# Kernel tuning notes

Hardware: AMD Instinct MI355X
Metric: run time of the kernel (lower is better)

The kernel has to match this reference:

```python
import jax, jax.numpy as jnp
import numpy as np

S = 16384   # num src nodes
D = 16384   # num dst nodes
FS = 128    # src feature len
FD = 128    # dst feature len
R = 50.0    # dist threshold (m)
L = 2005.0  # box side so avg degree ~ 32
LN_EPS = 1e-5


def setup_inputs() -> dict:
    rng = np.random.default_rng(0)
    src_pos_np = rng.uniform(0.0, L, (S, 2)).astype(np.float32)
    dst_pos_np = rng.uniform(0.0, L, (D, 2)).astype(np.float32)
    # radius-graph edge construction (data-dependent, done once outside jit)
    es, ed = [], []
    CH = 2048
    for i in range(0, S, CH):
        d = np.linalg.norm(src_pos_np[i:i + CH, None, :] - dst_pos_np[None, :, :], axis=-1)
        si, di = np.nonzero(d <= R)
        es.append((si + i).astype(np.int32))
        ed.append(di.astype(np.int32))
    edge_src_idx = jnp.asarray(np.concatenate(es))
    edge_dst_idx = jnp.asarray(np.concatenate(ed))

    key = jax.random.key(0)
    ks = jax.random.split(key, 12)
    w = lambda k, shape: (jax.random.normal(k, shape, jnp.float32) * 0.02)
    return {
        'src_node_features': jax.random.normal(ks[0], (S, FS), jnp.float32),
        'src_node_pos': jnp.asarray(src_pos_np),
        'dst_node_features': jax.random.normal(ks[1], (D, FD), jnp.float32),
        'dst_node_pos': jnp.asarray(dst_pos_np),
        'src_w': w(ks[2], (FS, FS)), 'src_b': jnp.zeros((FS,), jnp.float32),
        'dst_w': w(ks[3], (FD, FD)), 'dst_b': jnp.zeros((FD,), jnp.float32),
        'dist_w': w(ks[4], (2, FD)), 'dist_b': jnp.zeros((FD,), jnp.float32),
        'edge_w1': w(ks[5], (FS + FD + FD, FD)), 'edge_b1': jnp.zeros((FD,), jnp.float32),
        'edge_w2': w(ks[6], (FD, FD)), 'edge_b2': jnp.zeros((FD,), jnp.float32),
        'ln_g': jnp.ones((FD,), jnp.float32), 'ln_b': jnp.zeros((FD,), jnp.float32),
        'out_w': w(ks[7], (FD, FD)), 'out_b': jnp.zeros((FD,), jnp.float32),
        'edge_src_idx': edge_src_idx,
        'edge_dst_idx': edge_dst_idx,
    }


def reference(src_node_features, src_node_pos, dst_node_features, dst_node_pos,
              src_w, src_b, dst_w, dst_b, dist_w, dist_b,
              edge_w1, edge_b1, edge_w2, edge_b2, ln_g, ln_b, out_w, out_b,
              edge_src_idx, edge_dst_idx):
    # node encoders: Linear + ReLU
    src_enc = jax.nn.relu(src_node_features @ src_w + src_b)   # [S, FS]
    dst_enc = jax.nn.relu(dst_node_features @ dst_w + dst_b)   # [D, FD]
    # gather per-edge
    e_src = src_enc[edge_src_idx]                               # [E, FS]
    e_dst = dst_enc[edge_dst_idx]                               # [E, FD]
    e_dpos = src_node_pos[edge_src_idx] - dst_node_pos[edge_dst_idx]  # [E, 2]
    e_dist = jax.nn.relu(e_dpos @ dist_w + dist_b)              # [E, FD]
    # edge MLP: Linear-ReLU-Linear on concat [E, FS+FD+FD]
    e_in = jnp.concatenate([e_src, e_dist, e_dst], axis=-1)
    e_out = jax.nn.relu(e_in @ edge_w1 + edge_b1) @ edge_w2 + edge_b2  # [E, FD]
    # scatter-add to destination nodes
    agg = dst_enc + jax.ops.segment_sum(e_out, edge_dst_idx, num_segments=D)
    # LayerNorm + ReLU + Linear + residual + ReLU
    mu = jnp.mean(agg, axis=-1, keepdims=True)
    var = jnp.mean(jnp.square(agg - mu), axis=-1, keepdims=True)
    ln = (agg - mu) * jax.lax.rsqrt(var + LN_EPS) * ln_g + ln_b
    h = jax.nn.relu(ln) @ out_w + out_b + dst_node_features
    return jax.nn.relu(h)
```

## Files before the change

### kernel.cpp

```cpp
#include <hip/hip_runtime.h>

typedef unsigned short ushort_t;
typedef unsigned int uint_t;
typedef short bhalf8 __attribute__((ext_vector_type(8)));
typedef float f32x4 __attribute__((ext_vector_type(4)));

#define DEG_CAP 96
#define PWIN 192

__device__ __forceinline__ float b2f(ushort_t u) {
    union { uint_t i; float f; } v; v.i = ((uint_t)u) << 16; return v.f;
}
__device__ __forceinline__ float u2f(uint_t u) {
    union { uint_t i; float f; } v; v.i = u; return v.f;
}
__device__ __forceinline__ ushort_t f2b(float f) {
    union { float f; uint_t i; } v; v.f = f;
    uint_t r = v.i + 0x7fffu + ((v.i >> 16) & 1u);
    return (ushort_t)(r >> 16);
}
__device__ __forceinline__ uint_t f2u(float f) {
    union { float f; uint_t i; } v; v.f = f; return v.i;
}
__device__ __forceinline__ uint_t pack_trunc(float lo, float hi) {
    return (f2u(lo) >> 16) | (f2u(hi) & 0xffff0000u);
}
__device__ __forceinline__ uint_t addpack_trunc(uint_t a, uint_t b) {
    union { uint_t i; float f; } t0, t1, s0, s1;
    t0.i = a << 16;          s0.i = b << 16;
    t1.i = a & 0xffff0000u;  s1.i = b & 0xffff0000u;
    return pack_trunc(t0.f + s0.f, t1.f + s1.f);
}

__global__ __launch_bounds__(256) void prep_kernel(
    const float* __restrict__ wsrc, const float* __restrict__ wdst,
    const float* __restrict__ w2,   const float* __restrict__ wout,
    const float* __restrict__ w1,
    ushort_t* __restrict__ msrc, ushort_t* __restrict__ mdst,
    ushort_t* __restrict__ m2,   ushort_t* __restrict__ mout,
    ushort_t* __restrict__ m1a,  ushort_t* __restrict__ m1b,
    ushort_t* __restrict__ m1c,
    const int* __restrict__ esi, const int* __restrict__ edi, int E,
    int* __restrict__ deg, int* __restrict__ bucket,
    float* __restrict__ hsum, int countB, int zeroB, int Dn)
{
    int b = blockIdx.x, tid = threadIdx.x;
    if (b < 56) {
        const float* ins[7] = { wsrc, wdst, w2, wout, w1, w1 + 16384, w1 + 32768 };
        ushort_t* outs[7]   = { msrc, mdst, m2, mout, m1a, m1b, m1c };
        int mat = b >> 3;
        const float* in = ins[mat];
        ushort_t* out = outs[mat];
        int flat = (b & 7)*256 + tid;
        int nt = flat >> 8, rem = flat & 255;
        int ks = rem >> 6, lane = rem & 63;
        int q = lane >> 4, m = lane & 15;
        #pragma unroll
        for (int j = 0; j < 8; ++j)
            out[flat*8 + j] = f2b(in[(ks*32 + q*8 + j)*128 + nt*16 + m]);
    } else if (b < 56 + countB) {
        int i = (b - 56)*256 + tid;
        if (i < E) {
            int d = edi[i];
            int p = atomicAdd(&deg[d], 1);
            if (p < DEG_CAP) bucket[(size_t)d*DEG_CAP + p] = esi[i];
        }
    } else {
        int zb = b - 56 - countB;
        float4* h4 = (float4*)hsum;
        int total4 = Dn*32;
        for (int i = zb*256 + tid; i < total4; i += zeroB*256)
            h4[i] = make_float4(0.f, 0.f, 0.f, 0.f);
    }
}

__global__ __launch_bounds__(256) void enc2_kernel(
    const float* __restrict__ src_feat, const float* __restrict__ dst_feat,
    const ushort_t* __restrict__ msrc, const ushort_t* __restrict__ mdst,
    const ushort_t* __restrict__ m1a,  const ushort_t* __restrict__ m1c,
    const float* __restrict__ src_b,   const float* __restrict__ dst_b,
    const float* __restrict__ b1,
    ushort_t* __restrict__ Csrc, ushort_t* __restrict__ Cdst,
    ushort_t* __restrict__ dst_enc,
    const int* __restrict__ deg, int* __restrict__ P,
    int* __restrict__ tileStart, int nTiles, int Dn,
    int Sb, int Db)
{
    int tid = threadIdx.x, blk = blockIdx.x;

    if (blk == Sb + Db) {
        __shared__ int sums[256];
        int per = Dn >> 8;
        const int4* d4 = (const int4*)(deg + tid*per);
        int4 v[16]; int s = 0;
        #pragma unroll
        for (int k = 0; k < 16; ++k) {
            v[k] = d4[k];
            v[k].x = min(v[k].x, DEG_CAP); v[k].y = min(v[k].y, DEG_CAP);
            v[k].z = min(v[k].z, DEG_CAP); v[k].w = min(v[k].w, DEG_CAP);
            s += v[k].x + v[k].y + v[k].z + v[k].w;
        }
        sums[tid] = s;
        __syncthreads();
        for (int off = 1; off < 256; off <<= 1) {
            int x = (tid >= off) ? sums[tid - off] : 0;
            __syncthreads();
            sums[tid] += x;
            __syncthreads();
        }
        int run = sums[tid] - s;
        int4* n4 = (int4*)(P + tid*per);
        auto wt = [&](int start, int end, int d) {
            for (int tt = (start + 63) >> 6; tt*64 < end && tt < nTiles; ++tt)
                tileStart[tt] = d;
        };
        #pragma unroll
        for (int k = 0; k < 16; ++k) {
            int d0 = tid*per + k*4;
            int4 o; int st;
            st = run; o.x = run; run += v[k].x; wt(st, run, d0 + 0);
            st = run; o.y = run; run += v[k].y; wt(st, run, d0 + 1);
            st = run; o.z = run; run += v[k].z; wt(st, run, d0 + 2);
            st = run; o.w = run; run += v[k].w; wt(st, run, d0 + 3);
            n4[k] = o;
        }
        return;
    }

    __shared__ ushort_t A_l[64*136];
    __shared__ ushort_t E_l[64*136];
    __shared__ float b_l[128];
    __shared__ float b2_l[128];

    const float* A; const ushort_t *W1m, *W2m; const float* bias; const float* bias2;
    ushort_t *outC, *outEnc; int rowbase;
    if (blk < Sb) { A = src_feat; W1m = msrc; W2m = m1a; bias = src_b;
                    outC = Csrc; outEnc = nullptr; rowbase = blk*64; bias2 = nullptr; }
    else          { A = dst_feat; W1m = mdst; W2m = m1c; bias = dst_b;
                    outC = Cdst; outEnc = dst_enc; rowbase = (blk - Sb)*64; bias2 = b1; }

    const float4* A4 = (const float4*)A;
    for (int i = tid; i < 2048; i += 256) {
        int r = i >> 5, c = i & 31;
        float4 v = A4[(size_t)(rowbase + r)*32 + c];
        uint2 u;
        u.x = pack_trunc(v.x, v.y);
        u.y = pack_trunc(v.z, v.w);
        *(uint2*)(A_l + r*136 + c*4) = u;
    }
    if (tid < 128) { b_l[tid] = bias[tid]; b2_l[tid] = bias2 ? bias2[tid] : 0.f; }
    __syncthreads();

    int lane = tid & 63, w = tid >> 6, q = lane >> 4, m = lane & 15;
    const bhalf8* Wv1 = (const bhalf8*)W1m;
    f32x4 acc[4][2] = {};
    #pragma unroll
    for (int ks = 0; ks < 4; ++ks) {
        bhalf8 bf0 = Wv1[((2*w)*4 + ks)*64 + lane];
        bhalf8 bf1 = Wv1[((2*w+1)*4 + ks)*64 + lane];
        #pragma unroll
        for (int mt = 0; mt < 4; ++mt) {
            bhalf8 a = *(const bhalf8*)(A_l + (mt*16 + m)*136 + ks*32 + q*8);
            acc[mt][0] = __builtin_amdgcn_mfma_f32_16x16x32_bf16(a, bf0, acc[mt][0], 0, 0, 0);
            acc[mt][1] = __builtin_amdgcn_mfma_f32_16x16x32_bf16(a, bf1, acc[mt][1], 0, 0, 0);
        }
    }
    #pragma unroll
    for (int mt = 0; mt < 4; ++mt)
    #pragma unroll
    for (int nt = 0; nt < 2; ++nt)
    #pragma unroll
    for (int reg = 0; reg < 4; ++reg) {
        int col = w*32 + nt*16 + m;
        int row = mt*16 + q*4 + reg;
        E_l[row*136 + col] = f2b(fmaxf(acc[mt][nt][reg] + b_l[col], 0.f));
    }
    __syncthreads();

    if (outEnc) {
        for (int i = tid; i < 1024; i += 256) {
            int r = i >> 4, c = i & 15;
            ((uint4*)outEnc)[(size_t)(rowbase + r)*16 + c] = *(const uint4*)(E_l + r*136 + c*8);
        }
    }

    const bhalf8* Wv2 = (const bhalf8*)W2m;
    f32x4 acc2[4][2] = {};
    #pragma unroll
    for (int ks = 0; ks < 4; ++ks) {
        bhalf8 bf0 = Wv2[((2*w)*4 + ks)*64 + lane];
        bhalf8 bf1 = Wv2[((2*w+1)*4 + ks)*64 + lane];
        #pragma unroll
        for (int mt = 0; mt < 4; ++mt) {
            bhalf8 a = *(const bhalf8*)(E_l + (mt*16 + m)*136 + ks*32 + q*8);
            acc2[mt][0] = __builtin_amdgcn_mfma_f32_16x16x32_bf16(a, bf0, acc2[mt][0], 0, 0, 0);
            acc2[mt][1] = __builtin_amdgcn_mfma_f32_16x16x32_bf16(a, bf1, acc2[mt][1], 0, 0, 0);
        }
    }
    #pragma unroll
    for (int mt = 0; mt < 4; ++mt)
    #pragma unroll
    for (int nt = 0; nt < 2; ++nt)
    #pragma unroll
    for (int reg = 0; reg < 4; ++reg) {
        int col = w*32 + nt*16 + m;
        int row = mt*16 + q*4 + reg;
        A_l[row*136 + col] = f2b(acc2[mt][nt][reg] + b2_l[col]);
    }
    __syncthreads();
    for (int i = tid; i < 1024; i += 256) {
        int r = i >> 4, c = i & 15;
        ((uint4*)outC)[(size_t)(rowbase + r)*16 + c] = *(const uint4*)(A_l + r*136 + c*8);
    }
}

__global__ __launch_bounds__(512, 8) void edge_kernel(
    const ushort_t* __restrict__ Csrc, const ushort_t* __restrict__ Cdst,
    const float* __restrict__ src_pos, const float* __restrict__ dst_pos,
    const int* __restrict__ P, const int* __restrict__ tileStart,
    const int* __restrict__ bucket, int E, int Dn,
    const ushort_t* __restrict__ w1bm,
    const float* __restrict__ dist_w, const float* __restrict__ dist_b,
    float* __restrict__ hsum)
{
    __shared__ char pool[17408];
    __shared__ ushort_t G[64*136];
    __shared__ int Pw[PWIN];
    __shared__ int s_l[64], d_l[64], dofs_l[64];
    __shared__ uint_t bndmask[2];
    __shared__ float dx_l[64], dy_l[64];
    __shared__ float dw0_l[128], dw1_l[128], db_l[128];

    ushort_t* X  = (ushort_t*)pool;
    ushort_t* Hc = (ushort_t*)pool;

    int tid = threadIdx.x, blk = blockIdx.x;
    int d0 = tileStart[blk];

    if (tid < PWIN) Pw[tid] = (d0 + tid < Dn) ? P[d0 + tid] : 0x7fffffff;
    if (tid < 128) {
        dw0_l[tid] = dist_w[tid];
        dw1_l[tid] = dist_w[128 + tid];
        db_l[tid]  = dist_b[tid];
    }
    __syncthreads();

    if (tid < 64) {
        int g = blk*64 + tid;
        int s = 0, d = -1;
        float dx = 0.f, dy = 0.f;
        if (g < E) {
            int i = 0;
            while (i + 1 < PWIN && Pw[i + 1] <= g) ++i;
            int p;
            if (i == PWIN - 1) {
                int lo = d0 + PWIN - 1, hi = Dn - 1;
                while (lo < hi) {
                    int mid = (lo + hi + 1) >> 1;
                    if (P[mid] <= g) lo = mid; else hi = mid - 1;
                }
                d = lo; p = g - P[lo];
            } else {
                d = d0 + i; p = g - Pw[i];
            }
            s = bucket[(size_t)d*DEG_CAP + min(p, DEG_CAP - 1)];
            float2 sp = ((const float2*)src_pos)[s];
            float2 dp = ((const float2*)dst_pos)[d];
            dx = sp.x - dp.x; dy = sp.y - dp.y;
        }
        s_l[tid] = s; d_l[tid] = d;
        dofs_l[tid] = (d >= 0) ? d*128 : -1;
        dx_l[tid] = dx; dy_l[tid] = dy;
        int dd = d_l[tid];
        int dn = (tid < 63) ? d_l[tid + 1] : -2;
        bool bnd = ((tid & 15) == 15) || (dn != dd);
        unsigned long long mask = __ballot(bnd);
        if (tid == 0) { bndmask[0] = (uint_t)mask; bndmask[1] = (uint_t)(mask >> 32); }
    }
    __syncthreads();

    const uint4* cs4 = (const uint4*)Csrc;
    const uint4* cd4 = (const uint4*)Cdst;
    #pragma unroll
    for (int k = 0; k < 2; ++k) {
        int i = tid + k*512;
        int r = i >> 4, c = i & 15;
        uint4 a = cs4[(size_t)s_l[r]*16 + c];
        uint4 b = cd4[(size_t)max(d_l[r], 0)*16 + c];
        uint4 u;
        u.x = addpack_trunc(a.x, b.x);
        u.y = addpack_trunc(a.y, b.y);
        u.z = addpack_trunc(a.z, b.z);
        u.w = addpack_trunc(a.w, b.w);
        *(uint4*)(G + r*136 + c*8) = u;
    }
    for (int i = tid; i < 4096; i += 512) {
        int r = i >> 6, j2 = (i & 63)*2;
        float dx = dx_l[r], dy = dy_l[r];
        float v0 = fmaxf(fmaf(dx, dw0_l[j2],   fmaf(dy, dw1_l[j2],   db_l[j2])),   0.f);
        float v1 = fmaxf(fmaf(dx, dw0_l[j2+1], fmaf(dy, dw1_l[j2+1], db_l[j2+1])), 0.f);
        *(uint_t*)(X + r*136 + j2) = pack_trunc(v0, v1);
    }
    __syncthreads();

    int lane = tid & 63, w = tid >> 6, q = lane >> 4, m = lane & 15;
    f32x4 acc[4] = {};
    const bhalf8* Wv = (const bhalf8*)w1bm;
    #pragma unroll
    for (int ks = 0; ks < 4; ++ks) {
        bhalf8 bf = Wv[(w*4 + ks)*64 + lane];
        #pragma unroll
        for (int mt = 0; mt < 4; ++mt) {
            bhalf8 a = *(const bhalf8*)(X + (mt*16 + m)*136 + ks*32 + q*8);
            acc[mt] = __builtin_amdgcn_mfma_f32_16x16x32_bf16(a, bf, acc[mt], 0, 0, 0);
        }
    }
    __syncthreads();

    #pragma unroll
    for (int mt = 0; mt < 4; ++mt) {
        int col = w*16 + m;
        int row0 = mt*16 + q*4;
        uint2 u;
        u.x = pack_trunc(acc[mt][0], acc[mt][1]);
        u.y = pack_trunc(acc[mt][2], acc[mt][3]);
        *(uint2*)(Hc + col*68 + row0) = u;
    }
    __syncthreads();

    {
        int j = tid & 127, h = tid >> 7;
        uint_t mask = bndmask[h >> 1] >> ((h & 1)*16);
        const ushort_t* Hcol = Hc + j*68 + h*16;
        int rbase = h*16;
        float a = 0.f;
        #pragma unroll
        for (int k4 = 0; k4 < 4; ++k4) {
            uint2 hp = *(const uint2*)(Hcol + k4*4);
            float hv[4];
            hv[0] = u2f(hp.x << 16);
            hv[1] = u2f(hp.x & 0xffff0000u);
            hv[2] = u2f(hp.y << 16);
            hv[3] = u2f(hp.y & 0xffff0000u);
            #pragma unroll
            for (int t = 0; t < 4; ++t) {
                int r = rbase + k4*4 + t;
                float g = b2f(G[r*136 + j]);
                a += fmaxf(hv[t] + g, 0.f);
                if ((mask >> (k4*4 + t)) & 1u) {
                    int ofs = dofs_l[r];
                    if (ofs >= 0) atomicAdd(&hsum[(size_t)ofs + j], a);
                    a = 0.f;
                }
            }
        }
    }
}

__global__ __launch_bounds__(256) void aggfinal16_kernel(
    const float* __restrict__ hsum, const ushort_t* __restrict__ w2m,
    const float* __restrict__ b2, const int* __restrict__ deg,
    const ushort_t* __restrict__ dst_enc, const float* __restrict__ ln_g,
    const float* __restrict__ ln_b, const ushort_t* __restrict__ moutm,
    const float* __restrict__ out_b, const float* __restrict__ dst_feat,
    float* __restrict__ out)
{
    __shared__ ushort_t A_l[16*136];
    __shared__ ushort_t E2[16*136];
    __shared__ float ps[64], ps2[64];
    __shared__ float muv[16], invv[16];
    __shared__ float pb2[128], pg[128], plb[128], pob[128];
    __shared__ int dgl[16];

    int tid = threadIdx.x, blk = blockIdx.x;
    int lane = tid & 63, w = tid >> 6, q = lane >> 4, m = lane & 15;

    if (tid < 128) { pb2[tid] = b2[tid]; pg[tid] = ln_g[tid];
                     plb[tid] = ln_b[tid]; pob[tid] = out_b[tid]; }
    if (tid < 16) dgl[tid] = deg[blk*16 + tid];
    {
        int r = tid >> 4, c = tid & 15;
        const float4* hv4 = (const float4*)hsum;
        size_t base = (size_t)(blk*16 + r)*32 + c*2;
        float4 p0 = hv4[base], p1 = hv4[base + 1];
        uint4 u;
        u.x = pack_trunc(p0.x, p0.y);
        u.y = pack_trunc(p0.z, p0.w);
        u.z = pack_trunc(p1.x, p1.y);
        u.w = pack_trunc(p1.z, p1.w);
        *(uint4*)(A_l + r*136 + c*8) = u;
        *(uint4*)(E2 + r*136 + c*8) = ((const uint4*)dst_enc)[(size_t)(blk*16 + r)*16 + c];
    }
    __syncthreads();

    const bhalf8* Wv2 = (const bhalf8*)w2m;
    f32x4 acc[2] = {};
    #pragma unroll
    for (int ks = 0; ks < 4; ++ks) {
        bhalf8 bf0 = Wv2[((2*w)*4 + ks)*64 + lane];
        bhalf8 bf1 = Wv2[((2*w+1)*4 + ks)*64 + lane];
        bhalf8 a = *(const bhalf8*)(A_l + m*136 + ks*32 + q*8);
        acc[0] = __builtin_amdgcn_mfma_f32_16x16x32_bf16(a, bf0, acc[0], 0, 0, 0);
        acc[1] = __builtin_amdgcn_mfma_f32_16x16x32_bf16(a, bf1, acc[1], 0, 0, 0);
    }
    float y[2][4];
    #pragma unroll
    for (int nt = 0; nt < 2; ++nt)
    #pragma unroll
    for (int reg = 0; reg < 4; ++reg) {
        int col = w*32 + nt*16 + m;
        int rowl = q*4 + reg;
        y[nt][reg] = acc[nt][reg] + (float)dgl[rowl]*pb2[col] + b2f(E2[rowl*136 + col]);
    }
    float s[4], s2[4];
    #pragma unroll
    for (int reg = 0; reg < 4; ++reg) {
        s[reg]  = y[0][reg] + y[1][reg];
        s2[reg] = y[0][reg]*y[0][reg] + y[1][reg]*y[1][reg];
    }
    #pragma unroll
    for (int o = 1; o < 16; o <<= 1) {
        #pragma unroll
        for (int reg = 0; reg < 4; ++reg) {
            s[reg]  += __shfl_xor(s[reg],  o);
            s2[reg] += __shfl_xor(s2[reg], o);
        }
    }
    if (m == 0) {
        #pragma unroll
        for (int reg = 0; reg < 4; ++reg) {
            ps[(q*4 + reg)*4 + w]  = s[reg];
            ps2[(q*4 + reg)*4 + w] = s2[reg];
        }
    }
    __syncthreads();
    if (tid < 16) {
        float su = ps[tid*4] + ps[tid*4+1] + ps[tid*4+2] + ps[tid*4+3];
        float sq = ps2[tid*4] + ps2[tid*4+1] + ps2[tid*4+2] + ps2[tid*4+3];
        float mu = su / 128.f;
        float var = sq / 128.f - mu*mu;
        muv[tid] = mu;
        invv[tid] = 1.0f / sqrtf(var + 1e-5f);
    }
    __syncthreads();
    #pragma unroll
    for (int nt = 0; nt < 2; ++nt)
    #pragma unroll
    for (int reg = 0; reg < 4; ++reg) {
        int col = w*32 + nt*16 + m;
        int rowl = q*4 + reg;
        float v = (y[nt][reg] - muv[rowl])*invv[rowl]*pg[col] + plb[col];
        A_l[rowl*136 + col] = f2b(fmaxf(v, 0.f));
    }
    __syncthreads();

    const bhalf8* Wo = (const bhalf8*)moutm;
    f32x4 acc2[2] = {};
    #pragma unroll
    for (int ks = 0; ks < 4; ++ks) {
        bhalf8 bf0 = Wo[((2*w)*4 + ks)*64 + lane];
        bhalf8 bf1 = Wo[((2*w+1)*4 + ks)*64 + lane];
        bhalf8 a = *(const bhalf8*)(A_l + m*136 + ks*32 + q*8);
        acc2[0] = __builtin_amdgcn_mfma_f32_16x16x32_bf16(a, bf0, acc2[0], 0, 0, 0);
        acc2[1] = __builtin_amdgcn_mfma_f32_16x16x32_bf16(a, bf1, acc2[1], 0, 0, 0);
    }
    #pragma unroll
    for (int nt = 0; nt < 2; ++nt)
    #pragma unroll
    for (int reg = 0; reg < 4; ++reg) {
        int col = w*32 + nt*16 + m;
        size_t grow = (size_t)blk*16 + q*4 + reg;
        float v = acc2[nt][reg] + pob[col] + dst_feat[grow*128 + col];
        out[grow*128 + col] = fmaxf(v, 0.f);
    }
}

extern "C" void kernel_launch(void* const* d_in, const int* in_sizes, int n_in,
                              void* d_out, int out_size, void* d_ws, size_t ws_size,
                              hipStream_t stream)
{
    const float* src_feat = (const float*)d_in[0];
    const float* src_pos  = (const float*)d_in[1];
    const float* dst_feat = (const float*)d_in[2];
    const float* dst_pos  = (const float*)d_in[3];
    const float* src_w    = (const float*)d_in[4];
    const float* src_b    = (const float*)d_in[5];
    const float* dst_w    = (const float*)d_in[6];
    const float* dst_b    = (const float*)d_in[7];
    const float* dist_w   = (const float*)d_in[8];
    const float* dist_b   = (const float*)d_in[9];
    const float* w1       = (const float*)d_in[10];
    const float* b1       = (const float*)d_in[11];
    const float* w2       = (const float*)d_in[12];
    const float* b2       = (const float*)d_in[13];
    const float* ln_g     = (const float*)d_in[14];
    const float* ln_b     = (const float*)d_in[15];
    const float* out_w    = (const float*)d_in[16];
    const float* out_b    = (const float*)d_in[17];
    const int* esi        = (const int*)d_in[18];
    const int* edi        = (const int*)d_in[19];
    int E = in_sizes[18];
    int S = in_sizes[0] / 128;
    int D = in_sizes[2] / 128;
    int nTiles = (E + 63) / 64;

    char* ws = (char*)d_ws;
    size_t off = 0;
    auto alloc = [&](size_t bytes) { char* p = ws + off; off += (bytes + 511) & ~(size_t)511; return p; };
    ushort_t* Csrc    = (ushort_t*)alloc((size_t)S*128*2);
    ushort_t* Cdst    = (ushort_t*)alloc((size_t)D*128*2);
    ushort_t* dst_enc = (ushort_t*)alloc((size_t)D*128*2);
    float*    hsum    = (float*)   alloc((size_t)D*128*4);
    ushort_t* t_src   = (ushort_t*)alloc(128*128*2);
    ushort_t* t_dst   = (ushort_t*)alloc(128*128*2);
    ushort_t* t_w2    = (ushort_t*)alloc(128*128*2);
    ushort_t* t_out   = (ushort_t*)alloc(128*128*2);
    ushort_t* t_1a    = (ushort_t*)alloc(128*128*2);
    ushort_t* t_1b    = (ushort_t*)alloc(128*128*2);
    ushort_t* t_1c    = (ushort_t*)alloc(128*128*2);
    int*      deg     = (int*)     alloc((size_t)D*4);
    int*      P       = (int*)     alloc((size_t)D*4);
    int*      tileS   = (int*)     alloc((size_t)nTiles*4);
    int*      bucket  = (int*)     alloc((size_t)D*DEG_CAP*4);

    hipMemsetAsync(deg, 0, (size_t)D*4, stream);

    int countB = (E + 255)/256;
    int zeroB = 256;
    prep_kernel<<<56 + countB + zeroB, 256, 0, stream>>>(
        src_w, dst_w, w2, out_w, w1,
        t_src, t_dst, t_w2, t_out, t_1a, t_1b, t_1c,
        esi, edi, E, deg, bucket, hsum, countB, zeroB, D);

    int Sb = S/64, Db = D/64;
    enc2_kernel<<<Sb + Db + 1, 256, 0, stream>>>(
        src_feat, dst_feat, t_src, t_dst, t_1a, t_1c, src_b, dst_b, b1,
        Csrc, Cdst, dst_enc, deg, P, tileS, nTiles, D, Sb, Db);

    edge_kernel<<<nTiles, 512, 0, stream>>>(
        Csrc, Cdst, src_pos, dst_pos, P, tileS, bucket, E, D,
        t_1b, dist_w, dist_b, hsum);

    aggfinal16_kernel<<<D/16, 256, 0, stream>>>(
        hsum, t_w2, b2, deg, dst_enc, ln_g, ln_b,
        t_out, out_b, dst_feat, (float*)d_out);
}
```

Measured before the change: 212.1 us.

## Materialize per-edge CSR pairs and reduce edge segments with a one-hot MFMA

A new csr_kernel writes an explicit (src,dst) pair per sorted edge. This replaces the per-thread window search over P and tileStart inside edge_kernel. In edge_kernel, the serial per-column segmented sum with many atomics is replaced by a one-hot segment matrix multiplied against the ReLU'd hidden tile on MFMA, so there is one atomic per segment and column. It also vectorises the dist-feature and bf16 add paths. The cost is an extra kernel launch, an E-sized int2 buffer with its initialisation, and rounding the hidden values to bf16 before the reduction.

```diff
diff --git a/kernel.cpp b/kernel.cpp
--- a/kernel.cpp
+++ b/kernel.cpp
@@ -4,9 +4,9 @@
 typedef unsigned int uint_t;
 typedef short bhalf8 __attribute__((ext_vector_type(8)));
 typedef float f32x4 __attribute__((ext_vector_type(4)));
+typedef float f32x2 __attribute__((ext_vector_type(2)));
 
 #define DEG_CAP 96
-#define PWIN 192
 
 __device__ __forceinline__ float b2f(ushort_t u) {
     union { uint_t i; float f; } v; v.i = ((uint_t)u) << 16; return v.f;
@@ -26,10 +26,11 @@
     return (f2u(lo) >> 16) | (f2u(hi) & 0xffff0000u);
 }
 __device__ __forceinline__ uint_t addpack_trunc(uint_t a, uint_t b) {
-    union { uint_t i; float f; } t0, t1, s0, s1;
-    t0.i = a << 16;          s0.i = b << 16;
-    t1.i = a & 0xffff0000u;  s1.i = b & 0xffff0000u;
-    return pack_trunc(t0.f + s0.f, t1.f + s1.f);
+    f32x2 A, B;
+    A.x = u2f(a << 16); A.y = u2f(a & 0xffff0000u);
+    B.x = u2f(b << 16); B.y = u2f(b & 0xffff0000u);
+    f32x2 C = A + B;
+    return pack_trunc(C.x, C.y);
 }
 
 __global__ __launch_bounds__(256) void prep_kernel(
@@ -42,6 +43,7 @@
     ushort_t* __restrict__ m1c,
     const int* __restrict__ esi, const int* __restrict__ edi, int E,
     int* __restrict__ deg, int* __restrict__ bucket,
+    int2* __restrict__ edge_sd,
     float* __restrict__ hsum, int countB, int zeroB, int Dn)
 {
     int b = blockIdx.x, tid = threadIdx.x;
@@ -71,6 +73,9 @@
         int total4 = Dn*32;
         for (int i = zb*256 + tid; i < total4; i += zeroB*256)
             h4[i] = make_float4(0.f, 0.f, 0.f, 0.f);
+        uint2* e2 = (uint2*)edge_sd;
+        for (int i = zb*256 + tid; i < E; i += zeroB*256)
+            e2[i] = make_uint2(0u, 0xFFFFFFFFu);
     }
 }
 
@@ -83,8 +88,7 @@
     ushort_t* __restrict__ Csrc, ushort_t* __restrict__ Cdst,
     ushort_t* __restrict__ dst_enc,
     const int* __restrict__ deg, int* __restrict__ P,
-    int* __restrict__ tileStart, int nTiles, int Dn,
-    int Sb, int Db)
+    int Dn, int Sb, int Db)
 {
     int tid = threadIdx.x, blk = blockIdx.x;
 
@@ -110,18 +114,13 @@
         }
         int run = sums[tid] - s;
         int4* n4 = (int4*)(P + tid*per);
-        auto wt = [&](int start, int end, int d) {
-            for (int tt = (start + 63) >> 6; tt*64 < end && tt < nTiles; ++tt)
-                tileStart[tt] = d;
-        };
         #pragma unroll
         for (int k = 0; k < 16; ++k) {
-            int d0 = tid*per + k*4;
-            int4 o; int st;
-            st = run; o.x = run; run += v[k].x; wt(st, run, d0 + 0);
-            st = run; o.y = run; run += v[k].y; wt(st, run, d0 + 1);
-            st = run; o.z = run; run += v[k].z; wt(st, run, d0 + 2);
-            st = run; o.w = run; run += v[k].w; wt(st, run, d0 + 3);
+            int4 o;
+            o.x = run; run += v[k].x;
+            o.y = run; run += v[k].y;
+            o.z = run; run += v[k].z;
+            o.w = run; run += v[k].w;
             n4[k] = o;
         }
         return;
@@ -214,70 +213,79 @@
     }
 }
 
+__global__ __launch_bounds__(256) void csr_kernel(
+    const int* __restrict__ P, const int* __restrict__ deg,
+    const int* __restrict__ bucket, int2* __restrict__ edge_sd, int Dn)
+{
+    int t = blockIdx.x*256 + threadIdx.x;
+    int d = t >> 2, pl = t & 3;
+    if (d >= Dn) return;
+    int st = P[d];
+    int n = min(deg[d], DEG_CAP);
+    const int* bk = bucket + (size_t)d*DEG_CAP;
+    for (int p = pl; p < n; p += 4)
+        edge_sd[st + p] = make_int2(bk[p], d);
+}
+
 __global__ __launch_bounds__(512, 8) void edge_kernel(
     const ushort_t* __restrict__ Csrc, const ushort_t* __restrict__ Cdst,
     const float* __restrict__ src_pos, const float* __restrict__ dst_pos,
-    const int* __restrict__ P, const int* __restrict__ tileStart,
-    const int* __restrict__ bucket, int E, int Dn,
+    const int2* __restrict__ edge_sd, int E,
     const ushort_t* __restrict__ w1bm,
     const float* __restrict__ dist_w, const float* __restrict__ dist_b,
     float* __restrict__ hsum)
 {
-    __shared__ char pool[17408];
+    __shared__ char pool[18432];
     __shared__ ushort_t G[64*136];
-    __shared__ int Pw[PWIN];
-    __shared__ int s_l[64], d_l[64], dofs_l[64];
-    __shared__ uint_t bndmask[2];
-    __shared__ float dx_l[64], dy_l[64];
+    __shared__ __align__(16) ushort_t Smat[64*72];
+    __shared__ int s_l[64], d_l[64], segd[64];
+    __shared__ float2 dxy_l[64];
     __shared__ float dw0_l[128], dw1_l[128], db_l[128];
+    __shared__ int nseg_s;
 
     ushort_t* X  = (ushort_t*)pool;
-    ushort_t* Hc = (ushort_t*)pool;
+    ushort_t* Hb = (ushort_t*)pool;
 
     int tid = threadIdx.x, blk = blockIdx.x;
-    int d0 = tileStart[blk];
-
-    if (tid < PWIN) Pw[tid] = (d0 + tid < Dn) ? P[d0 + tid] : 0x7fffffff;
+
+    {
+        uint4* sz = (uint4*)Smat;
+        if (tid < 576) sz[tid] = make_uint4(0u, 0u, 0u, 0u);
+        int i1 = tid + 512;
+        if (i1 < 576) sz[i1] = make_uint4(0u, 0u, 0u, 0u);
+    }
     if (tid < 128) {
         dw0_l[tid] = dist_w[tid];
         dw1_l[tid] = dist_w[128 + tid];
         db_l[tid]  = dist_b[tid];
     }
-    __syncthreads();
-
+
+    int segreg = 0;
     if (tid < 64) {
         int g = blk*64 + tid;
         int s = 0, d = -1;
         float dx = 0.f, dy = 0.f;
         if (g < E) {
-            int i = 0;
-            while (i + 1 < PWIN && Pw[i + 1] <= g) ++i;
-            int p;
-            if (i == PWIN - 1) {
-                int lo = d0 + PWIN - 1, hi = Dn - 1;
-                while (lo < hi) {
-                    int mid = (lo + hi + 1) >> 1;
-                    if (P[mid] <= g) lo = mid; else hi = mid - 1;
-                }
-                d = lo; p = g - P[lo];
-            } else {
-                d = d0 + i; p = g - Pw[i];
+            int2 sd = edge_sd[g];
+            if (sd.y >= 0) {
+                s = sd.x; d = sd.y;
+                float2 sp = ((const float2*)src_pos)[s];
+                float2 dp = ((const float2*)dst_pos)[d];
+                dx = sp.x - dp.x; dy = sp.y - dp.y;
             }
-            s = bucket[(size_t)d*DEG_CAP + min(p, DEG_CAP - 1)];
-            float2 sp = ((const float2*)src_pos)[s];
-            float2 dp = ((const float2*)dst_pos)[d];
-            dx = sp.x - dp.x; dy = sp.y - dp.y;
         }
         s_l[tid] = s; d_l[tid] = d;
-        dofs_l[tid] = (d >= 0) ? d*128 : -1;
-        dx_l[tid] = dx; dy_l[tid] = dy;
-        int dd = d_l[tid];
-        int dn = (tid < 63) ? d_l[tid + 1] : -2;
-        bool bnd = ((tid & 15) == 15) || (dn != dd);
-        unsigned long long mask = __ballot(bnd);
-        if (tid == 0) { bndmask[0] = (uint_t)mask; bndmask[1] = (uint_t)(mask >> 32); }
-    }
-    __syncthreads();
+        dxy_l[tid] = make_float2(dx, dy);
+        int dprev = __shfl_up(d, 1);
+        bool st = (tid == 0) || (d != dprev);
+        unsigned long long smask = __ballot(st);
+        segreg = (int)__popcll(smask << (63 - tid)) - 1;
+        if (st) segd[segreg] = (d >= 0) ? d*128 : -1;
+        if (tid == 0) nseg_s = (int)__popcll(smask);
+    }
+    __syncthreads();
+
+    if (tid < 64) Smat[segreg*72 + tid] = (ushort_t)0x3f80;
 
     const uint4* cs4 = (const uint4*)Csrc;
     const uint4* cd4 = (const uint4*)Cdst;
@@ -294,12 +302,21 @@
         u.w = addpack_trunc(a.w, b.w);
         *(uint4*)(G + r*136 + c*8) = u;
     }
-    for (int i = tid; i < 4096; i += 512) {
-        int r = i >> 6, j2 = (i & 63)*2;
-        float dx = dx_l[r], dy = dy_l[r];
-        float v0 = fmaxf(fmaf(dx, dw0_l[j2],   fmaf(dy, dw1_l[j2],   db_l[j2])),   0.f);
-        float v1 = fmaxf(fmaf(dx, dw0_l[j2+1], fmaf(dy, dw1_l[j2+1], db_l[j2+1])), 0.f);
-        *(uint_t*)(X + r*136 + j2) = pack_trunc(v0, v1);
+
+    {
+        int j2 = (tid & 63)*2;
+        int r0 = tid >> 6;
+        float w00 = dw0_l[j2], w01 = dw0_l[j2+1];
+        float w10 = dw1_l[j2], w11 = dw1_l[j2+1];
+        float bb0 = db_l[j2],  bb1 = db_l[j2+1];
+        #pragma unroll
+        for (int k = 0; k < 8; ++k) {
+            int r = r0 + k*8;
+            float2 dd = dxy_l[r];
+            float v0 = fmaxf(fmaf(dd.x, w00, fmaf(dd.y, w10, bb0)), 0.f);
+            float v1 = fmaxf(fmaf(dd.x, w01, fmaf(dd.y, w11, bb1)), 0.f);
+            *(uint_t*)(X + r*136 + j2) = pack_trunc(v0, v1);
+        }
     }
     __syncthreads();
 
@@ -317,41 +334,38 @@
     }
     __syncthreads();
 
+    int col = w*16 + m;
     #pragma unroll
     for (int mt = 0; mt < 4; ++mt) {
-        int col = w*16 + m;
         int row0 = mt*16 + q*4;
+        float v0 = fmaxf(acc[mt][0] + b2f(G[(row0+0)*136 + col]), 0.f);
+        float v1 = fmaxf(acc[mt][1] + b2f(G[(row0+1)*136 + col]), 0.f);
+        float v2 = fmaxf(acc[mt][2] + b2f(G[(row0+2)*136 + col]), 0.f);
+        float v3 = fmaxf(acc[mt][3] + b2f(G[(row0+3)*136 + col]), 0.f);
         uint2 u;
-        u.x = pack_trunc(acc[mt][0], acc[mt][1]);
-        u.y = pack_trunc(acc[mt][2], acc[mt][3]);
-        *(uint2*)(Hc + col*68 + row0) = u;
-    }
-    __syncthreads();
-
-    {
-        int j = tid & 127, h = tid >> 7;
-        uint_t mask = bndmask[h >> 1] >> ((h & 1)*16);
-        const ushort_t* Hcol = Hc + j*68 + h*16;
-        int rbase = h*16;
-        float a = 0.f;
-        #pragma unroll
-        for (int k4 = 0; k4 < 4; ++k4) {
-            uint2 hp = *(const uint2*)(Hcol + k4*4);
-            float hv[4];
-            hv[0] = u2f(hp.x << 16);
-            hv[1] = u2f(hp.x & 0xffff0000u);
-            hv[2] = u2f(hp.y << 16);
-            hv[3] = u2f(hp.y & 0xffff0000u);
-            #pragma unroll
-            for (int t = 0; t < 4; ++t) {
-                int r = rbase + k4*4 + t;
-                float g = b2f(G[r*136 + j]);
-                a += fmaxf(hv[t] + g, 0.f);
-                if ((mask >> (k4*4 + t)) & 1u) {
-                    int ofs = dofs_l[r];
-                    if (ofs >= 0) atomicAdd(&hsum[(size_t)ofs + j], a);
-                    a = 0.f;
-                }
+        u.x = (uint_t)f2b(v0) | ((uint_t)f2b(v1) << 16);
+        u.y = (uint_t)f2b(v2) | ((uint_t)f2b(v3) << 16);
+        *(uint2*)(Hb + col*72 + row0) = u;
+    }
+    __syncthreads();
+
+    int ns = nseg_s;
+    const ushort_t* hrow = Hb + col*72 + q*8;
+    bhalf8 hb0 = *(const bhalf8*)(hrow);
+    bhalf8 hb1 = *(const bhalf8*)(hrow + 32);
+    for (int sb = 0; sb*16 < ns; ++sb) {
+        const ushort_t* srow = Smat + (sb*16 + m)*72 + q*8;
+        bhalf8 a0 = *(const bhalf8*)(srow);
+        bhalf8 a1 = *(const bhalf8*)(srow + 32);
+        f32x4 o = {};
+        o = __builtin_amdgcn_mfma_f32_16x16x32_bf16(a0, hb0, o, 0, 0, 0);
+        o = __builtin_amdgcn_mfma_f32_16x16x32_bf16(a1, hb1, o, 0, 0, 0);
+        #pragma unroll
+        for (int reg = 0; reg < 4; ++reg) {
+            int seg = sb*16 + q*4 + reg;
+            if (seg < ns) {
+                int ofs = segd[seg];
+                if (ofs >= 0) atomicAdd(&hsum[(size_t)ofs + col], o[reg]);
             }
         }
     }
@@ -520,8 +534,8 @@
     ushort_t* t_1c    = (ushort_t*)alloc(128*128*2);
     int*      deg     = (int*)     alloc((size_t)D*4);
     int*      P       = (int*)     alloc((size_t)D*4);
-    int*      tileS   = (int*)     alloc((size_t)nTiles*4);
     int*      bucket  = (int*)     alloc((size_t)D*DEG_CAP*4);
+    int2*     edge_sd = (int2*)    alloc((size_t)E*8);
 
     hipMemsetAsync(deg, 0, (size_t)D*4, stream);
 
@@ -530,15 +544,17 @@
     prep_kernel<<<56 + countB + zeroB, 256, 0, stream>>>(
         src_w, dst_w, w2, out_w, w1,
         t_src, t_dst, t_w2, t_out, t_1a, t_1b, t_1c,
-        esi, edi, E, deg, bucket, hsum, countB, zeroB, D);
+        esi, edi, E, deg, bucket, edge_sd, hsum, countB, zeroB, D);
 
     int Sb = S/64, Db = D/64;
     enc2_kernel<<<Sb + Db + 1, 256, 0, stream>>>(
         src_feat, dst_feat, t_src, t_dst, t_1a, t_1c, src_b, dst_b, b1,
-        Csrc, Cdst, dst_enc, deg, P, tileS, nTiles, D, Sb, Db);
+        Csrc, Cdst, dst_enc, deg, P, D, Sb, Db);
+
+    csr_kernel<<<(D*4 + 255)/256, 256, 0, stream>>>(P, deg, bucket, edge_sd, D);
 
     edge_kernel<<<nTiles, 512, 0, stream>>>(
-        Csrc, Cdst, src_pos, dst_pos, P, tileS, bucket, E, D,
+        Csrc, Cdst, src_pos, dst_pos, edge_sd, E,
         t_1b, dist_w, dist_b, hsum);
 
     aggfinal16_kernel<<<D/16, 256, 0, stream>>>(
```

New measurement: 207.9 us. 2.0% less time.
